# Kernel optimization log

Hardware: AMD Instinct MI355X
Metric: run time of the kernel (lower is better)

## Reference

```python
import jax, jax.numpy as jnp
import numpy as np

NUM_USERS = 1_000_000
NUM_ITEMS = 500_000
NUM_GENRES = 20
NUM_TAGS = 100
EMBEDDING_DIM = 64
HIDDEN_UNITS = [256, 128, 64]
NUM_CLASSES = 5
BATCH = 16384


def setup_inputs() -> dict:
    key = jax.random.key(0)
    ks = jax.random.split(key, 16)
    deep_in = EMBEDDING_DIM * 2 + NUM_GENRES + NUM_TAGS  # 248
    inp = {
        "user": jax.random.randint(ks[0], (BATCH,), 0, NUM_USERS),
        "item": jax.random.randint(ks[1], (BATCH,), 0, NUM_ITEMS),
        "genre": jax.random.uniform(ks[2], (BATCH, NUM_GENRES), dtype=jnp.float32),
        "tag": jax.random.uniform(ks[3], (BATCH, NUM_TAGS), dtype=jnp.float32),
        # wide Linear(num_users+num_items -> HIDDEN_UNITS[-1]); stored transposed
        # as (vocab, out) so the one-hot matmul becomes a row gather.
        "wide_W": jax.random.normal(ks[4], (NUM_USERS + NUM_ITEMS, HIDDEN_UNITS[-1]), dtype=jnp.float32) * 0.01,
        "wide_b": jnp.zeros((HIDDEN_UNITS[-1],), dtype=jnp.float32),
        "user_emb": jax.random.normal(ks[5], (NUM_USERS, EMBEDDING_DIM), dtype=jnp.float32) * 0.01,
        "item_emb": jax.random.normal(ks[6], (NUM_ITEMS, EMBEDDING_DIM), dtype=jnp.float32) * 0.01,
        "W0": jax.random.normal(ks[7], (deep_in, HIDDEN_UNITS[0]), dtype=jnp.float32) * 0.02,
        "b0": jnp.zeros((HIDDEN_UNITS[0],), dtype=jnp.float32),
        "W1": jax.random.normal(ks[8], (HIDDEN_UNITS[0], HIDDEN_UNITS[1]), dtype=jnp.float32) * 0.02,
        "b1": jnp.zeros((HIDDEN_UNITS[1],), dtype=jnp.float32),
        "W2": jax.random.normal(ks[9], (HIDDEN_UNITS[1], HIDDEN_UNITS[2]), dtype=jnp.float32) * 0.02,
        "b2": jnp.zeros((HIDDEN_UNITS[2],), dtype=jnp.float32),
        "final_W": jax.random.normal(ks[10], (HIDDEN_UNITS[-1] * 2, NUM_CLASSES), dtype=jnp.float32) * 0.02,
        "final_b": jnp.zeros((NUM_CLASSES,), dtype=jnp.float32),
    }
    return inp


def reference(user, item, genre, tag, wide_W, wide_b, user_emb, item_emb,
              W0, b0, W1, b1, W2, b2, final_W, final_b):
    # Wide path: one_hot(user)++one_hot(item) @ W + b  ==  gather+sum of rows.
    wide_out = wide_W[user] + wide_W[NUM_USERS + item] + wide_b  # [B, 64]
    # Deep path (dropout is identity in eval mode).
    u = user_emb[user]   # [B, E]
    v = item_emb[item]   # [B, E]
    h = jnp.concatenate([u, v, genre, tag], axis=1)  # [B, 248]
    h = jax.nn.relu(h @ W0 + b0)
    h = jax.nn.relu(h @ W1 + b1)
    h = jax.nn.relu(h @ W2 + b2)  # [B, 64]
    combined = jnp.concatenate([h, wide_out], axis=1)  # [B, 128]
    logits = combined @ final_W + final_b  # [B, NUM_CLASSES]
    return logits
```

## Files before the change

kernel.cpp:

```cpp
#include <hip/hip_runtime.h>

#define BATCH 16384
#define NU 1000000
#define TBR 64
#define MT 512
#define WSOFF0 0
#define WSOFF1 65536
#define WSOFF2 98304
#define WSREQ  212992

typedef __attribute__((ext_vector_type(8))) short short8;
typedef __attribute__((ext_vector_type(4))) short short4v;
typedef __attribute__((ext_vector_type(4))) float f32x4;

__device__ __forceinline__ unsigned short f32_bf16(float f) {
    unsigned int u = __float_as_uint(f);
    u += 0x7FFF + ((u >> 16) & 1);
    return (unsigned short)(u >> 16);
}
__device__ __forceinline__ float bf16_f32(unsigned short h) {
    return __uint_as_float(((unsigned int)h) << 16);
}

__device__ __forceinline__ int swz(int row, int byteInRow, int rowStrideB) {
    return row * rowStrideB + (byteInRow ^ ((row & 7) << 4));
}

__device__ __forceinline__ short8 cvt8(float4 a, float4 b) {
    short8 s;
    s[0] = (short)f32_bf16(a.x); s[1] = (short)f32_bf16(a.y);
    s[2] = (short)f32_bf16(a.z); s[3] = (short)f32_bf16(a.w);
    s[4] = (short)f32_bf16(b.x); s[5] = (short)f32_bf16(b.y);
    s[6] = (short)f32_bf16(b.z); s[7] = (short)f32_bf16(b.w);
    return s;
}

__global__ void prep_weights(const float* __restrict__ W0, const float* __restrict__ W1,
                             const float* __restrict__ W2, unsigned short* __restrict__ ws)
{
    __shared__ float t[32 * 65];
    int b = blockIdx.x;
    const float* src; unsigned short* dst; int K, N, K2, k0, n0;
    if (b < 32)      { src = W0; dst = ws + WSOFF0; K = 248; N = 256; K2 = 256; k0 = (b >> 2) * 32; n0 = (b & 3) * 64; }
    else if (b < 48) { int i = b - 32; src = W1; dst = ws + WSOFF1; K = 256; N = 128; K2 = 256; k0 = (i >> 1) * 32; n0 = (i & 1) * 64; }
    else             { int i = b - 48; src = W2; dst = ws + WSOFF2; K = 128; N = 64;  K2 = 128; k0 = i * 32; n0 = 0; }

    int tid = threadIdx.x;
    for (int q = tid; q < 32 * 16; q += 256) {
        int k = q >> 4, nq = q & 15;
        float4 v = make_float4(0.f, 0.f, 0.f, 0.f);
        if (k0 + k < K) v = *(const float4*)(src + (size_t)(k0 + k) * N + n0 + nq * 4);
        t[k * 65 + nq * 4 + 0] = v.x;
        t[k * 65 + nq * 4 + 1] = v.y;
        t[k * 65 + nq * 4 + 2] = v.z;
        t[k * 65 + nq * 4 + 3] = v.w;
    }
    __syncthreads();
    {
        int q = tid;
        int n = q >> 2, kg = q & 3;
        short8 o;
        #pragma unroll
        for (int i = 0; i < 8; ++i) o[i] = (short)f32_bf16(t[(kg * 8 + i) * 65 + n]);
        *(short8*)(dst + (size_t)(n0 + n) * K2 + k0 + kg * 8) = o;
    }
}

__global__ __launch_bounds__(MT, 1) void wd_mfma(
        const int* __restrict__ user, const int* __restrict__ item,
        const float* __restrict__ genre, const float* __restrict__ tag,
        const float* __restrict__ wide_W, const float* __restrict__ wide_b,
        const float* __restrict__ user_emb, const float* __restrict__ item_emb,
        const float* __restrict__ b0, const float* __restrict__ b1,
        const float* __restrict__ b2,
        const float* __restrict__ fW, const float* __restrict__ fb,
        const unsigned short* __restrict__ ws, float* __restrict__ out)
{
    __shared__ unsigned short sX[TBR * 256];
    __shared__ unsigned short sH0[TBR * 256];
    __shared__ unsigned short sH1[TBR * 128];
    __shared__ unsigned short sH2[TBR * 72];
    __shared__ unsigned short sWide[TBR * 72];
    __shared__ float sFW[640];

    const int tid = threadIdx.x;
    const int row0 = blockIdx.x * TBR;
    const unsigned short* w0t = ws + WSOFF0;
    const unsigned short* w1t = ws + WSOFF1;
    const unsigned short* w2t = ws + WSOFF2;

    const int wid = tid >> 6;
    const int lane = tid & 63;
    const int lr = lane & 15;
    const int lh = lane >> 4;

    const int cb0 = wid * 32;
    const int cb1 = wid * 16;
    const int cb2 = (wid & 3) * 16;
    short8 B0[2][8];
    #pragma unroll
    for (int t = 0; t < 2; ++t)
        #pragma unroll
        for (int kc = 0; kc < 8; ++kc)
            B0[t][kc] = *(const short8*)(w0t + (size_t)(cb0 + t * 16 + lr) * 256 + kc * 32 + lh * 8);
    short8 B1[8];
    #pragma unroll
    for (int kc = 0; kc < 8; ++kc)
        B1[kc] = *(const short8*)(w1t + (size_t)(cb1 + lr) * 256 + kc * 32 + lh * 8);
    short8 B2f[4];
    #pragma unroll
    for (int kc = 0; kc < 4; ++kc)
        B2f[kc] = *(const short8*)(w2t + (size_t)(cb2 + lr) * 128 + kc * 32 + lh * 8);
    float rb0[2];
    rb0[0] = b0[cb0 + lr]; rb0[1] = b0[cb0 + 16 + lr];
    float rb1 = b1[cb1 + lr];
    float rb2 = b2[cb2 + lr];

    #pragma unroll
    for (int it = 0; it < 6; ++it) {
        int q = tid + it * MT;
        if (it < 4) {
            int r = q >> 5, j = q & 31;
            int grow = row0 + r;
            float4 va = make_float4(0.f, 0.f, 0.f, 0.f);
            float4 vb = va;
            if (j < 8) {
                const float4* p = (const float4*)(user_emb + (size_t)user[grow] * 64);
                va = p[j * 2]; vb = p[j * 2 + 1];
            } else if (j < 16) {
                const float4* p = (const float4*)(item_emb + (size_t)item[grow] * 64);
                va = p[(j - 8) * 2]; vb = p[(j - 8) * 2 + 1];
            } else if (j == 16) {
                const float4* p = (const float4*)(genre + (size_t)grow * 20);
                va = p[0]; vb = p[1];
            } else if (j == 17) {
                const float4* p = (const float4*)(genre + (size_t)grow * 20);
                va = p[2]; vb = p[3];
            } else if (j == 18) {
                va = *(const float4*)(genre + (size_t)grow * 20 + 16);
                vb = *(const float4*)(tag + (size_t)grow * 100);
            } else if (j < 31) {
                const float4* p = (const float4*)(tag + (size_t)grow * 100 + 4);
                int jj = j - 19;
                va = p[jj * 2]; vb = p[jj * 2 + 1];
            }
            *(short8*)((char*)sX + swz(r, j * 16, 512)) = cvt8(va, vb);
        } else {
            int p = q - 4 * MT;
            int r = p >> 4, j = p & 15;
            int grow = row0 + r;
            float4 a = ((const float4*)(wide_W + (size_t)user[grow] * 64))[j];
            float4 b = ((const float4*)(wide_W + (size_t)(NU + item[grow]) * 64))[j];
            float4 c = ((const float4*)wide_b)[j];
            short4v o;
            o[0] = (short)f32_bf16(a.x + b.x + c.x);
            o[1] = (short)f32_bf16(a.y + b.y + c.y);
            o[2] = (short)f32_bf16(a.z + b.z + c.z);
            o[3] = (short)f32_bf16(a.w + b.w + c.w);
            *(short4v*)(sWide + r * 72 + j * 4) = o;
        }
    }
    if (tid < 160) {
        ((float4*)sFW)[tid] = ((const float4*)fW)[tid];
    }
    __syncthreads();

    {
        f32x4 acc[4][2];
        #pragma unroll
        for (int rt = 0; rt < 4; ++rt)
            #pragma unroll
            for (int t = 0; t < 2; ++t) acc[rt][t] = (f32x4)(0.f);

        #pragma unroll
        for (int kc = 0; kc < 8; ++kc) {
            const int kb = kc * 32 + lh * 8;
            short8 a[4];
            #pragma unroll
            for (int rt = 0; rt < 4; ++rt)
                a[rt] = *(const short8*)((const char*)sX + swz(rt * 16 + lr, kb * 2, 512));
            #pragma unroll
            for (int t = 0; t < 2; ++t)
                #pragma unroll
                for (int rt = 0; rt < 4; ++rt)
                    acc[rt][t] = __builtin_amdgcn_mfma_f32_16x16x32_bf16(a[rt], B0[t][kc], acc[rt][t], 0, 0, 0);
        }
        #pragma unroll
        for (int t = 0; t < 2; ++t) {
            #pragma unroll
            for (int rt = 0; rt < 4; ++rt)
                #pragma unroll
                for (int jj = 0; jj < 4; ++jj) {
                    int row = rt * 16 + lh * 4 + jj;
                    float v = fmaxf(acc[rt][t][jj] + rb0[t], 0.f);
                    *(unsigned short*)((char*)sH0 + swz(row, (cb0 + t * 16 + lr) * 2, 512)) = f32_bf16(v);
                }
        }
        __syncthreads();
    }

    {
        f32x4 acc[4];
        #pragma unroll
        for (int rt = 0; rt < 4; ++rt) acc[rt] = (f32x4)(0.f);

        #pragma unroll
        for (int kc = 0; kc < 8; ++kc) {
            const int kb = kc * 32 + lh * 8;
            short8 a[4];
            #pragma unroll
            for (int rt = 0; rt < 4; ++rt)
                a[rt] = *(const short8*)((const char*)sH0 + swz(rt * 16 + lr, kb * 2, 512));
            #pragma unroll
            for (int rt = 0; rt < 4; ++rt)
                acc[rt] = __builtin_amdgcn_mfma_f32_16x16x32_bf16(a[rt], B1[kc], acc[rt], 0, 0, 0);
        }
        #pragma unroll
        for (int rt = 0; rt < 4; ++rt)
            #pragma unroll
            for (int jj = 0; jj < 4; ++jj) {
                int row = rt * 16 + lh * 4 + jj;
                float v = fmaxf(acc[rt][jj] + rb1, 0.f);
                *(unsigned short*)((char*)sH1 + swz(row, (cb1 + lr) * 2, 256)) = f32_bf16(v);
            }
        __syncthreads();
    }

    {
        const int rtb = (wid >> 2) * 2;
        f32x4 acc[2];
        acc[0] = (f32x4)(0.f); acc[1] = (f32x4)(0.f);

        #pragma unroll
        for (int kc = 0; kc < 4; ++kc) {
            const int kb = kc * 32 + lh * 8;
            #pragma unroll
            for (int rr = 0; rr < 2; ++rr) {
                short8 a = *(const short8*)((const char*)sH1 + swz((rtb + rr) * 16 + lr, kb * 2, 256));
                acc[rr] = __builtin_amdgcn_mfma_f32_16x16x32_bf16(a, B2f[kc], acc[rr], 0, 0, 0);
            }
        }
        #pragma unroll
        for (int rr = 0; rr < 2; ++rr)
            #pragma unroll
            for (int jj = 0; jj < 4; ++jj) {
                int row = (rtb + rr) * 16 + lh * 4 + jj;
                sH2[row * 72 + cb2 + lr] = f32_bf16(fmaxf(acc[rr][jj] + rb2, 0.f));
            }
        __syncthreads();
    }

    if (tid < TBR * 5) {
        int r = tid / 5, c = tid - r * 5;
        float acc = fb[c];
        #pragma unroll
        for (int kq = 0; kq < 8; ++kq) {
            short8 h = *(const short8*)(sH2 + r * 72 + kq * 8);
            #pragma unroll
            for (int i = 0; i < 8; ++i)
                acc = fmaf(bf16_f32((unsigned short)h[i]), sFW[(kq * 8 + i) * 5 + c], acc);
        }
        #pragma unroll
        for (int kq = 0; kq < 8; ++kq) {
            short8 h = *(const short8*)(sWide + r * 72 + kq * 8);
            #pragma unroll
            for (int i = 0; i < 8; ++i)
                acc = fmaf(bf16_f32((unsigned short)h[i]), sFW[(64 + kq * 8 + i) * 5 + c], acc);
        }
        out[(size_t)(row0 + r) * 5 + c] = acc;
    }
}

#define NTHR 256
#define TB 32

__device__ __forceinline__ void fma4(float4& a, float s, const float4& w) {
    a.x = fmaf(s, w.x, a.x); a.y = fmaf(s, w.y, a.y);
    a.z = fmaf(s, w.z, a.z); a.w = fmaf(s, w.w, a.w);
}
__device__ __forceinline__ float4 add4(const float4& a, const float4& b) {
    return make_float4(a.x + b.x, a.y + b.y, a.z + b.z, a.w + b.w);
}
__device__ __forceinline__ float4 relu4(const float4& a) {
    return make_float4(fmaxf(a.x, 0.f), fmaxf(a.y, 0.f), fmaxf(a.z, 0.f), fmaxf(a.w, 0.f));
}

__global__ void wd_fused(const int* __restrict__ user, const int* __restrict__ item,
                         const float* __restrict__ genre, const float* __restrict__ tag,
                         const float* __restrict__ wide_W, const float* __restrict__ wide_b,
                         const float* __restrict__ user_emb, const float* __restrict__ item_emb,
                         const float* __restrict__ W0, const float* __restrict__ b0,
                         const float* __restrict__ W1, const float* __restrict__ b1,
                         const float* __restrict__ W2, const float* __restrict__ b2,
                         const float* __restrict__ fW, const float* __restrict__ fb,
                         float* __restrict__ out)
{
    __shared__ float sA[TB * 248];
    __shared__ float sB[TB * 256];
    __shared__ float sC[TB * 64];

    const int tid = threadIdx.x;
    const int row0 = blockIdx.x * TB;

    for (int q = tid; q < TB * 62; q += NTHR) {
        int r = q / 62, j = q - r * 62, grow = row0 + r;
        float4 v;
        if (j < 16) v = reinterpret_cast<const float4*>(user_emb + (size_t)user[grow] * 64)[j];
        else if (j < 32) v = reinterpret_cast<const float4*>(item_emb + (size_t)item[grow] * 64)[j - 16];
        else if (j < 37) v = reinterpret_cast<const float4*>(genre + (size_t)grow * 20)[j - 32];
        else v = reinterpret_cast<const float4*>(tag + (size_t)grow * 100)[j - 37];
        *reinterpret_cast<float4*>(sA + r * 248 + j * 4) = v;
    }
    for (int q = tid; q < TB * 16; q += NTHR) {
        int r = q >> 4, j = q & 15, grow = row0 + r;
        float4 a = reinterpret_cast<const float4*>(wide_W + (size_t)user[grow] * 64)[j];
        float4 b = reinterpret_cast<const float4*>(wide_W + (size_t)(NU + item[grow]) * 64)[j];
        float4 c = reinterpret_cast<const float4*>(wide_b)[j];
        *reinterpret_cast<float4*>(sC + r * 64 + j * 4) =
            make_float4(a.x + b.x + c.x, a.y + b.y + c.y, a.z + b.z + c.z, a.w + b.w + c.w);
    }
    __syncthreads();
    {
        const int cg = tid & 63, r0 = (tid >> 6) * 8;
        float4 acc[8];
        #pragma unroll
        for (int r = 0; r < 8; ++r) acc[r] = make_float4(0.f, 0.f, 0.f, 0.f);
        for (int k = 0; k < 248; k += 4) {
            const float4* wp = reinterpret_cast<const float4*>(W0 + (size_t)k * 256) + cg;
            float4 w0 = wp[0], w1 = wp[64], w2 = wp[128], w3 = wp[192];
            #pragma unroll
            for (int r = 0; r < 8; ++r) {
                float4 xv = *reinterpret_cast<const float4*>(sA + (r0 + r) * 248 + k);
                fma4(acc[r], xv.x, w0); fma4(acc[r], xv.y, w1);
                fma4(acc[r], xv.z, w2); fma4(acc[r], xv.w, w3);
            }
        }
        float4 bb = reinterpret_cast<const float4*>(b0)[cg];
        #pragma unroll
        for (int r = 0; r < 8; ++r)
            *reinterpret_cast<float4*>(sB + (r0 + r) * 256 + cg * 4) = relu4(add4(acc[r], bb));
    }
    __syncthreads();
    {
        const int cg = tid & 31, r0 = (tid >> 5) * 4;
        float4 acc[4];
        #pragma unroll
        for (int r = 0; r < 4; ++r) acc[r] = make_float4(0.f, 0.f, 0.f, 0.f);
        for (int k = 0; k < 256; k += 4) {
            const float4* wp = reinterpret_cast<const float4*>(W1 + (size_t)k * 128) + cg;
            float4 w0 = wp[0], w1 = wp[32], w2 = wp[64], w3 = wp[96];
            #pragma unroll
            for (int r = 0; r < 4; ++r) {
                float4 xv = *reinterpret_cast<const float4*>(sB + (r0 + r) * 256 + k);
                fma4(acc[r], xv.x, w0); fma4(acc[r], xv.y, w1);
                fma4(acc[r], xv.z, w2); fma4(acc[r], xv.w, w3);
            }
        }
        float4 bb = reinterpret_cast<const float4*>(b1)[cg];
        #pragma unroll
        for (int r = 0; r < 4; ++r)
            *reinterpret_cast<float4*>(sA + (r0 + r) * 128 + cg * 4) = relu4(add4(acc[r], bb));
    }
    __syncthreads();
    {
        const int cg = tid & 15, r0 = (tid >> 4) * 2;
        float4 acc[2];
        acc[0] = make_float4(0.f, 0.f, 0.f, 0.f); acc[1] = acc[0];
        for (int k = 0; k < 128; k += 4) {
            const float4* wp = reinterpret_cast<const float4*>(W2 + (size_t)k * 64) + cg;
            float4 w0 = wp[0], w1 = wp[16], w2 = wp[32], w3 = wp[48];
            #pragma unroll
            for (int r = 0; r < 2; ++r) {
                float4 xv = *reinterpret_cast<const float4*>(sA + (r0 + r) * 128 + k);
                fma4(acc[r], xv.x, w0); fma4(acc[r], xv.y, w1);
                fma4(acc[r], xv.z, w2); fma4(acc[r], xv.w, w3);
            }
        }
        float4 bb = reinterpret_cast<const float4*>(b2)[cg];
        #pragma unroll
        for (int r = 0; r < 2; ++r)
            *reinterpret_cast<float4*>(sB + (r0 + r) * 64 + cg * 4) = relu4(add4(acc[r], bb));
    }
    __syncthreads();
    if (tid < TB * 5) {
        int r = tid / 5, c = tid - r * 5;
        float acc = fb[c];
        for (int k = 0; k < 64; ++k) acc = fmaf(sB[r * 64 + k], fW[k * 5 + c], acc);
        for (int k = 0; k < 64; ++k) acc = fmaf(sC[r * 64 + k], fW[(64 + k) * 5 + c], acc);
        out[(size_t)(row0 + r) * 5 + c] = acc;
    }
}

extern "C" void kernel_launch(void* const* d_in, const int* in_sizes, int n_in,
                              void* d_out, int out_size, void* d_ws, size_t ws_size,
                              hipStream_t stream) {
    const int* user = (const int*)d_in[0];
    const int* item = (const int*)d_in[1];
    const float* genre = (const float*)d_in[2];
    const float* tag = (const float*)d_in[3];
    const float* wide_W = (const float*)d_in[4];
    const float* wide_b = (const float*)d_in[5];
    const float* user_emb = (const float*)d_in[6];
    const float* item_emb = (const float*)d_in[7];
    const float* W0 = (const float*)d_in[8];
    const float* b0 = (const float*)d_in[9];
    const float* W1 = (const float*)d_in[10];
    const float* b1 = (const float*)d_in[11];
    const float* W2 = (const float*)d_in[12];
    const float* b2 = (const float*)d_in[13];
    const float* fW = (const float*)d_in[14];
    const float* fb = (const float*)d_in[15];
    float* out = (float*)d_out;

    if (ws_size >= (size_t)WSREQ) {
        hipLaunchKernelGGL(prep_weights, dim3(52), dim3(256), 0, stream,
                           W0, W1, W2, (unsigned short*)d_ws);
        hipLaunchKernelGGL(wd_mfma, dim3(BATCH / TBR), dim3(MT), 0, stream,
                           user, item, genre, tag, wide_W, wide_b, user_emb, item_emb,
                           b0, b1, b2, fW, fb, (const unsigned short*)d_ws, out);
    } else {
        hipLaunchKernelGGL(wd_fused, dim3(BATCH / TB), dim3(NTHR), 0, stream,
                           user, item, genre, tag, wide_W, wide_b, user_emb, item_emb,
                           W0, b0, W1, b1, W2, b2, fW, fb, out);
    }
}
```

Before: 30.86 us.

## Split MLP layers into row halves and interleave across layers

Each MLP layer is now processed in two 32-row halves. Layer L+1 on the first half is interleaved with layer L on the second half, so each barrier interval holds independent MFMA work from two layers. The barrier count goes from four to five, but the waits between dependent layers become shorter and there is more instruction-level overlap. Accumulator register pressure also drops.

```diff
diff --git a/kernel.cpp b/kernel.cpp
--- a/kernel.cpp
+++ b/kernel.cpp
@@ -97,6 +97,7 @@
     const int cb0 = wid * 32;
     const int cb1 = wid * 16;
     const int cb2 = (wid & 3) * 16;
+    const int rq2 = (wid >> 2) * 16;
     short8 B0[2][8];
     #pragma unroll
     for (int t = 0; t < 2; ++t)
@@ -163,92 +164,91 @@
     if (tid < 160) {
         ((float4*)sFW)[tid] = ((const float4*)fW)[tid];
     }
-    __syncthreads();
-
-    {
-        f32x4 acc[4][2];
-        #pragma unroll
-        for (int rt = 0; rt < 4; ++rt)
+
+    auto do_L0 = [&](int h) {
+        const int rb = h * 32;
+        f32x4 acc[2][2];
+        #pragma unroll
+        for (int rt = 0; rt < 2; ++rt)
             #pragma unroll
             for (int t = 0; t < 2; ++t) acc[rt][t] = (f32x4)(0.f);
-
         #pragma unroll
         for (int kc = 0; kc < 8; ++kc) {
             const int kb = kc * 32 + lh * 8;
-            short8 a[4];
-            #pragma unroll
-            for (int rt = 0; rt < 4; ++rt)
-                a[rt] = *(const short8*)((const char*)sX + swz(rt * 16 + lr, kb * 2, 512));
+            short8 a[2];
+            #pragma unroll
+            for (int rt = 0; rt < 2; ++rt)
+                a[rt] = *(const short8*)((const char*)sX + swz(rb + rt * 16 + lr, kb * 2, 512));
             #pragma unroll
             for (int t = 0; t < 2; ++t)
                 #pragma unroll
-                for (int rt = 0; rt < 4; ++rt)
+                for (int rt = 0; rt < 2; ++rt)
                     acc[rt][t] = __builtin_amdgcn_mfma_f32_16x16x32_bf16(a[rt], B0[t][kc], acc[rt][t], 0, 0, 0);
         }
         #pragma unroll
-        for (int t = 0; t < 2; ++t) {
-            #pragma unroll
-            for (int rt = 0; rt < 4; ++rt)
+        for (int t = 0; t < 2; ++t)
+            #pragma unroll
+            for (int rt = 0; rt < 2; ++rt)
                 #pragma unroll
                 for (int jj = 0; jj < 4; ++jj) {
-                    int row = rt * 16 + lh * 4 + jj;
+                    int row = rb + rt * 16 + lh * 4 + jj;
                     float v = fmaxf(acc[rt][t][jj] + rb0[t], 0.f);
                     *(unsigned short*)((char*)sH0 + swz(row, (cb0 + t * 16 + lr) * 2, 512)) = f32_bf16(v);
                 }
-        }
-        __syncthreads();
-    }
-
-    {
-        f32x4 acc[4];
-        #pragma unroll
-        for (int rt = 0; rt < 4; ++rt) acc[rt] = (f32x4)(0.f);
-
+    };
+
+    auto do_L1 = [&](int h) {
+        const int rb = h * 32;
+        f32x4 acc[2];
+        acc[0] = (f32x4)(0.f); acc[1] = (f32x4)(0.f);
         #pragma unroll
         for (int kc = 0; kc < 8; ++kc) {
             const int kb = kc * 32 + lh * 8;
-            short8 a[4];
-            #pragma unroll
-            for (int rt = 0; rt < 4; ++rt)
-                a[rt] = *(const short8*)((const char*)sH0 + swz(rt * 16 + lr, kb * 2, 512));
-            #pragma unroll
-            for (int rt = 0; rt < 4; ++rt)
+            short8 a[2];
+            #pragma unroll
+            for (int rt = 0; rt < 2; ++rt)
+                a[rt] = *(const short8*)((const char*)sH0 + swz(rb + rt * 16 + lr, kb * 2, 512));
+            #pragma unroll
+            for (int rt = 0; rt < 2; ++rt)
                 acc[rt] = __builtin_amdgcn_mfma_f32_16x16x32_bf16(a[rt], B1[kc], acc[rt], 0, 0, 0);
         }
         #pragma unroll
-        for (int rt = 0; rt < 4; ++rt)
+        for (int rt = 0; rt < 2; ++rt)
             #pragma unroll
             for (int jj = 0; jj < 4; ++jj) {
-                int row = rt * 16 + lh * 4 + jj;
+                int row = rb + rt * 16 + lh * 4 + jj;
                 float v = fmaxf(acc[rt][jj] + rb1, 0.f);
                 *(unsigned short*)((char*)sH1 + swz(row, (cb1 + lr) * 2, 256)) = f32_bf16(v);
             }
-        __syncthreads();
-    }
-
-    {
-        const int rtb = (wid >> 2) * 2;
-        f32x4 acc[2];
-        acc[0] = (f32x4)(0.f); acc[1] = (f32x4)(0.f);
-
+    };
+
+    auto do_L2 = [&](int h) {
+        const int rb = h * 32 + rq2;
+        f32x4 acc = (f32x4)(0.f);
         #pragma unroll
         for (int kc = 0; kc < 4; ++kc) {
             const int kb = kc * 32 + lh * 8;
-            #pragma unroll
-            for (int rr = 0; rr < 2; ++rr) {
-                short8 a = *(const short8*)((const char*)sH1 + swz((rtb + rr) * 16 + lr, kb * 2, 256));
-                acc[rr] = __builtin_amdgcn_mfma_f32_16x16x32_bf16(a, B2f[kc], acc[rr], 0, 0, 0);
-            }
-        }
-        #pragma unroll
-        for (int rr = 0; rr < 2; ++rr)
-            #pragma unroll
-            for (int jj = 0; jj < 4; ++jj) {
-                int row = (rtb + rr) * 16 + lh * 4 + jj;
-                sH2[row * 72 + cb2 + lr] = f32_bf16(fmaxf(acc[rr][jj] + rb2, 0.f));
-            }
-        __syncthreads();
-    }
+            short8 a = *(const short8*)((const char*)sH1 + swz(rb + lr, kb * 2, 256));
+            acc = __builtin_amdgcn_mfma_f32_16x16x32_bf16(a, B2f[kc], acc, 0, 0, 0);
+        }
+        #pragma unroll
+        for (int jj = 0; jj < 4; ++jj) {
+            int row = rb + lh * 4 + jj;
+            sH2[row * 72 + cb2 + lr] = f32_bf16(fmaxf(acc[jj] + rb2, 0.f));
+        }
+    };
+
+    __syncthreads();
+    do_L0(0);
+    __syncthreads();
+    do_L0(1);
+    do_L1(0);
+    __syncthreads();
+    do_L1(1);
+    do_L2(0);
+    __syncthreads();
+    do_L2(1);
+    __syncthreads();
 
     if (tid < TBR * 5) {
         int r = tid / 5, c = tid - r * 5;
```

After: 30.38 us. About the same (-1.5%).
